# Optimization experiments

Measured on AMD Instinct MI355X. Metric: run time of the kernel, lower is better.

Reference implementation:

```python
import jax, jax.numpy as jnp
import numpy as np

N, E, H, HEADS, NC, BLK = 100000, 1600000, 128, 4, 8192, 128

def _layernorm(x, g, b, eps=1e-5):
    m = jnp.mean(x, axis=-1, keepdims=True)
    v = jnp.var(x, axis=-1, keepdims=True)
    return (x - m) * jax.lax.rsqrt(v + eps) * g + b

def setup_inputs() -> dict:
    key = jax.random.key(0)
    ks = jax.random.split(key, 24)
    s = 0.05
    p = lambda k, shp: jax.random.normal(k, shp, jnp.float32) * s
    return {
        'x': jax.random.normal(ks[0], (N, H), jnp.float32),
        'ea': jax.random.normal(ks[1], (E, H), jnp.float32),
        # GINEConv edge linear (edge_dim -> hidden)
        'We': p(ks[2], (H, H)), 'be_': p(ks[3], (H,)),
        # GINEConv mlp: Linear(H,H) -> ReLU -> Linear(H,H)
        'W1': p(ks[4], (H, H)), 'b1': p(ks[5], (H,)),
        'W2': p(ks[6], (H, H)), 'b2': p(ks[7], (H,)),
        'ln1_g': jnp.ones((H,), jnp.float32), 'ln1_b': jnp.zeros((H,), jnp.float32),
        # MultiheadAttention packed qkv + out proj
        'in_w': p(ks[8], (3 * H, H)), 'in_b': p(ks[9], (3 * H,)),
        'out_w': p(ks[10], (H, H)), 'out_b': p(ks[11], (H,)),
        'ln2_g': jnp.ones((H,), jnp.float32), 'ln2_b': jnp.zeros((H,), jnp.float32),
        # FFN: Linear(H,2H) -> ReLU -> Linear(2H,H)
        'f1_w': p(ks[12], (2 * H, H)), 'f1_b': p(ks[13], (2 * H,)),
        'f2_w': p(ks[14], (H, 2 * H)), 'f2_b': p(ks[15], (H,)),
        'ei': jax.random.randint(ks[16], (2, E), 0, N, jnp.int64),
        'chem_idx': jnp.arange(NC, dtype=jnp.int64),
        'B': BLK,
    }

def reference(x, ea, We, be_, W1, b1, W2, b2, ln1_g, ln1_b, in_w, in_b,
              out_w, out_b, ln2_g, ln2_b, f1_w, f1_b, f2_w, f2_b,
              ei, chem_idx, B):
    n = x.shape[0]
    # ---- GINEConv: out_i = mlp((1+eps)*x_i + sum_j relu(x_j + lin(e_ji))), eps=0 ----
    src, dst = ei[0], ei[1]
    msg = jax.nn.relu(x[src] + ea @ We.T + be_)          # [E, H]
    agg = jax.ops.segment_sum(msg, dst, num_segments=n)  # [N, H]
    h = agg + x
    h = jax.nn.relu(h @ W1.T + b1) @ W2.T + b2
    x = _layernorm(x + h, ln1_g, ln1_b)
    # ---- chunked self-attention over chem nodes (chunks of size B) ----
    xc = x[chem_idx].reshape(-1, B, x.shape[-1])         # [nc, B, H]
    nc, _, hid = xc.shape
    dh = hid // HEADS
    qkv = xc @ in_w.T + in_b                             # [nc, B, 3H]
    q, k, v = jnp.split(qkv, 3, axis=-1)
    sp = lambda t: t.reshape(nc, B, HEADS, dh)
    att = jax.nn.softmax(jnp.einsum('bqhd,bkhd->bhqk', sp(q), sp(k)) * (1.0 / np.sqrt(dh)).astype(np.float32), axis=-1)
    o = jnp.einsum('bhqk,bkhd->bqhd', att, sp(v)).reshape(nc, B, hid)
    xc = xc + (o @ out_w.T + out_b)                      # residual inside BlockMHA
    xc = xc.reshape(-1, hid)
    # ---- FFN on chem subset ----
    h2 = _layernorm(xc, ln2_g, ln2_b)
    xc = xc + (jax.nn.relu(h2 @ f1_w.T + f1_b) @ f2_w.T + f2_b)
    return x.at[chem_idx].set(xc)
```

## Files before the change

kernel.cpp:

```cpp
#include <hip/hip_runtime.h>
#include <hip/hip_bf16.h>
#include <math.h>

typedef __attribute__((ext_vector_type(8))) __bf16 bf16x8;
typedef __attribute__((ext_vector_type(4))) float f32x4;
typedef __attribute__((ext_vector_type(4))) unsigned short u16x4;

#define HD  128
#define LDP 136

__device__ __forceinline__ unsigned short f2bf(float f) {
  __bf16 h = (__bf16)f;
  union { __bf16 h; unsigned short u; } v; v.h = h; return v.u;
}
__device__ __forceinline__ float bf2f(unsigned short h) {
  union { unsigned u; float f; } v; v.u = ((unsigned)h) << 16; return v.f;
}

__device__ __forceinline__ int idx_at(const void* p, long long i, int is64) {
  if (is64) return (int)((const long long*)p)[i];
  return ((const int*)p)[i];
}

__device__ __forceinline__ void mfma_tile_128(const unsigned short* a_s,
                                              const unsigned short* w_s,
                                              int w, int l15, int lg,
                                              f32x4 acc[2][8]) {
#pragma unroll
  for (int kk = 0; kk < 4; ++kk) {
    bf16x8 a[2], b[8];
#pragma unroll
    for (int mt = 0; mt < 2; ++mt)
      a[mt] = *(const bf16x8*)&a_s[(w * 32 + mt * 16 + l15) * LDP + kk * 32 + lg * 8];
#pragma unroll
    for (int nt = 0; nt < 8; ++nt)
      b[nt] = *(const bf16x8*)&w_s[(nt * 16 + l15) * LDP + kk * 32 + lg * 8];
#pragma unroll
    for (int mt = 0; mt < 2; ++mt)
#pragma unroll
      for (int nt = 0; nt < 8; ++nt)
        acc[mt][nt] = __builtin_amdgcn_mfma_f32_16x16x32_bf16(a[mt], b[nt], acc[mt][nt], 0, 0, 0);
  }
}

__device__ __forceinline__ void mfma_tile_gb(const unsigned short* a_s,
                                             const unsigned short* Wb,
                                             int w, int l15, int lg,
                                             f32x4 acc[2][8]) {
#pragma unroll
  for (int kk = 0; kk < 4; ++kk) {
    bf16x8 a[2], b[8];
#pragma unroll
    for (int mt = 0; mt < 2; ++mt)
      a[mt] = *(const bf16x8*)&a_s[(w * 32 + mt * 16 + l15) * LDP + kk * 32 + lg * 8];
#pragma unroll
    for (int nt = 0; nt < 8; ++nt)
      b[nt] = *(const bf16x8*)&Wb[(nt * 16 + l15) * 128 + kk * 32 + lg * 8];
#pragma unroll
    for (int mt = 0; mt < 2; ++mt)
#pragma unroll
      for (int nt = 0; nt < 8; ++nt)
        acc[mt][nt] = __builtin_amdgcn_mfma_f32_16x16x32_bf16(a[mt], b[nt], acc[mt][nt], 0, 0, 0);
  }
}

__device__ __forceinline__ void stage_f32s(unsigned short* dst, const float* src,
                                           long long src_ld, int tid, int T) {
  for (int i = tid; i < 128 * 32; i += T) {
    int r = i >> 5, c = (i & 31) << 2;
    float4 f = *(const float4*)&src[(long long)r * src_ld + c];
    u16x4 h = { f2bf(f.x), f2bf(f.y), f2bf(f.z), f2bf(f.w) };
    *(u16x4*)&dst[r * LDP + c] = h;
  }
}

__global__ void detect_idx_kernel(const void* __restrict__ ei, int E, int N,
                                  int* __restrict__ flag) {
  if (threadIdx.x == 0 && blockIdx.x == 0) {
    const long long* p = (const long long*)ei;
    int is64 = 1;
    long long step = E / 64; if (step < 1) step = 1;
    for (int i = 0; i < 64; ++i) {
      long long v = p[i * step];
      if (v < 0 || v >= N) { is64 = 0; break; }
    }
    *flag = is64;
  }
}

__global__ __launch_bounds__(256) void conv_we_kernel(const float* __restrict__ We,
                                                      unsigned short* __restrict__ we_bf) {
  int i = blockIdx.x * 256 + threadIdx.x;
  if (i < 128 * 128) {
    int r = i >> 7, c = i & 127;
    we_bf[r * 136 + c] = f2bf(We[i]);
  }
}
__global__ __launch_bounds__(256) void conv_w_kernel(const float* __restrict__ W,
                                                     unsigned short* __restrict__ out,
                                                     int n) {
  int i = blockIdx.x * 256 + threadIdx.x;
  if (i < n) out[i] = f2bf(W[i]);
}
__global__ __launch_bounds__(256) void conv_x_kernel(const float* __restrict__ x,
                                                     unsigned short* __restrict__ xb,
                                                     long long n8) {
  long long i = blockIdx.x * 256LL + threadIdx.x;
  if (i < n8) {
    float4 f0 = *(const float4*)&x[i * 8];
    float4 f1 = *(const float4*)&x[i * 8 + 4];
    u16x4 h0 = { f2bf(f0.x), f2bf(f0.y), f2bf(f0.z), f2bf(f0.w) };
    u16x4 h1 = { f2bf(f1.x), f2bf(f1.y), f2bf(f1.z), f2bf(f1.w) };
    *(u16x4*)&xb[i * 8] = h0;
    *(u16x4*)&xb[i * 8 + 4] = h1;
  }
}

__global__ __launch_bounds__(256) void hist_kernel(const void* __restrict__ ei,
                                                   const int* __restrict__ flag,
                                                   int* __restrict__ deg, int E) {
  const int is64 = *flag;
  for (long long e = blockIdx.x * 256LL + threadIdx.x; e < E;
       e += (long long)gridDim.x * 256)
    atomicAdd(&deg[idx_at(ei, (long long)E + e, is64)], 1);
}

#define SCH 1024
__global__ __launch_bounds__(256) void scan_a(const int* __restrict__ deg,
                                              int* __restrict__ bsum, int N) {
  const int b = blockIdx.x, t = threadIdx.x;
  int p = 0;
#pragma unroll
  for (int k = 0; k < 4; ++k) {
    int idx = b * SCH + t * 4 + k;
    if (idx < N) p += deg[idx];
  }
  __shared__ int warr[4];
  for (int o = 32; o > 0; o >>= 1) p += __shfl_xor(p, o);
  if ((t & 63) == 0) warr[t >> 6] = p;
  __syncthreads();
  if (t == 0) bsum[b] = warr[0] + warr[1] + warr[2] + warr[3];
}
__global__ void scan_b(int* __restrict__ bsum, int* __restrict__ off, int NB, int N) {
  if (threadIdx.x == 0 && blockIdx.x == 0) {
    int run = 0;
    for (int b = 0; b < NB; ++b) { int t = bsum[b]; bsum[b] = run; run += t; }
    off[N] = run;
  }
}
__global__ __launch_bounds__(128) void scan_b2(int* __restrict__ bsum,
                                               int* __restrict__ off, int NB, int N) {
  __shared__ int arr[128];
  const int t = threadIdx.x;
  int v = (t < NB) ? bsum[t] : 0;
  arr[t] = v;
  __syncthreads();
  for (int s = 1; s < 128; s <<= 1) {
    int u = (t >= s) ? arr[t - s] : 0;
    __syncthreads();
    arr[t] += u;
    __syncthreads();
  }
  if (t < NB) bsum[t] = arr[t] - v;
  if (t == 0) off[N] = arr[127];
}
__global__ __launch_bounds__(256) void scan_c(const int* __restrict__ deg,
                                              const int* __restrict__ bsum,
                                              int* __restrict__ off,
                                              int* __restrict__ cursor, int N) {
  const int b = blockIdx.x, t = threadIdx.x;
  int d[4], s = 0;
#pragma unroll
  for (int k = 0; k < 4; ++k) {
    int idx = b * SCH + t * 4 + k;
    d[k] = (idx < N) ? deg[idx] : 0;
    s += d[k];
  }
  __shared__ int arr[256];
  arr[t] = s;
  __syncthreads();
  for (int stp = 1; stp < 256; stp <<= 1) {
    int v = (t >= stp) ? arr[t - stp] : 0;
    __syncthreads();
    arr[t] += v;
    __syncthreads();
  }
  int base = bsum[b] + arr[t] - s;
  int acc = 0;
#pragma unroll
  for (int k = 0; k < 4; ++k) {
    int idx = b * SCH + t * 4 + k;
    if (idx < N) { off[idx] = base + acc; cursor[idx] = base + acc; }
    acc += d[k];
  }
}

__global__ __launch_bounds__(256, 4) void edge_kernel9(
    const unsigned short* __restrict__ x_bf, const float* __restrict__ ea,
    const unsigned short* __restrict__ we_bf, const float* __restrict__ be,
    const void* __restrict__ ei, const int* __restrict__ flag,
    int* __restrict__ cursor, unsigned short* __restrict__ msg, int E) {
  __shared__ unsigned short we_s[128 * LDP];
  __shared__ int s_src[128];
  __shared__ int s_pos[128];
  const int tid = threadIdx.x;
  const long long e0 = (long long)blockIdx.x * 128;
  const int is64 = *flag;

  if (tid < 128) {
    long long e = e0 + tid;
    int s = 0, p = 0;
    if (e < E) {
      s = idx_at(ei, e, is64);
      int d = idx_at(ei, (long long)E + e, is64);
      p = atomicAdd(&cursor[d], 1);
    }
    s_src[tid] = s; s_pos[tid] = p;
  }

  const int lane = tid & 63, w = tid >> 6;
  const int l15 = lane & 15, lg = lane >> 4;

  float4 af[2][4][2];
#pragma unroll
  for (int mt = 0; mt < 2; ++mt) {
    long long row = e0 + w * 32 + mt * 16 + l15;
    const float* src = &ea[(row < E ? row : e0) * HD + lg * 8];
#pragma unroll
    for (int kk = 0; kk < 4; ++kk) {
      af[mt][kk][0] = *(const float4*)&src[kk * 32];
      af[mt][kk][1] = *(const float4*)&src[kk * 32 + 4];
    }
  }

  for (int i = tid; i < 2048; i += 256) {
    int r = i >> 4, c = (i & 15) << 3;
    *(float4*)&we_s[r * LDP + c] = *(const float4*)&we_bf[r * 136 + c];
  }

  bf16x8 a[2][4];
#pragma unroll
  for (int mt = 0; mt < 2; ++mt)
#pragma unroll
    for (int kk = 0; kk < 4; ++kk) {
      float4 f0 = af[mt][kk][0], f1 = af[mt][kk][1];
      bf16x8 t;
      t[0] = (__bf16)f0.x; t[1] = (__bf16)f0.y; t[2] = (__bf16)f0.z; t[3] = (__bf16)f0.w;
      t[4] = (__bf16)f1.x; t[5] = (__bf16)f1.y; t[6] = (__bf16)f1.z; t[7] = (__bf16)f1.w;
      a[mt][kk] = t;
    }
  __syncthreads();

  f32x4 acc[2][8];
#pragma unroll
  for (int mt = 0; mt < 2; ++mt)
#pragma unroll
    for (int nt = 0; nt < 8; ++nt) acc[mt][nt] = (f32x4){0.f, 0.f, 0.f, 0.f};

#pragma unroll
  for (int kk = 0; kk < 4; ++kk) {
    bf16x8 b[8];
#pragma unroll
    for (int nt = 0; nt < 8; ++nt)
      b[nt] = *(const bf16x8*)&we_s[(nt * 16 + l15) * LDP + kk * 32 + lg * 8];
#pragma unroll
    for (int mt = 0; mt < 2; ++mt)
#pragma unroll
      for (int nt = 0; nt < 8; ++nt)
        acc[mt][nt] = __builtin_amdgcn_mfma_f32_16x16x32_bf16(a[mt][kk], b[nt], acc[mt][nt], 0, 0, 0);
  }

  float bev[8];
#pragma unroll
  for (int nt = 0; nt < 8; ++nt) bev[nt] = be[nt * 16 + l15];
  __syncthreads();

#pragma unroll
  for (int mt = 0; mt < 2; ++mt)
#pragma unroll
    for (int r = 0; r < 4; ++r) {
      int m = w * 32 + mt * 16 + lg * 4 + r;
#pragma unroll
      for (int nt = 0; nt < 8; ++nt)
        we_s[m * LDP + nt * 16 + l15] = f2bf(acc[mt][nt][r] + bev[nt]);
    }
  __syncthreads();

  for (int i = tid; i < 128 * 16; i += 256) {
    int r = i >> 4, sg = i & 15;
    if (e0 + r >= E) continue;
    bf16x8 xv = *(const bf16x8*)&x_bf[(size_t)s_src[r] * HD + sg * 8];
    bf16x8 g = *(const bf16x8*)&we_s[r * LDP + sg * 8];
    u16x4 h0, h1;
#pragma unroll
    for (int k = 0; k < 4; ++k) {
      float v = (float)g[k] + (float)xv[k];
      h0[k] = f2bf(v > 0.f ? v : 0.f);
    }
#pragma unroll
    for (int k = 0; k < 4; ++k) {
      float v = (float)g[4 + k] + (float)xv[4 + k];
      h1[k] = f2bf(v > 0.f ? v : 0.f);
    }
    unsigned short* mp = &msg[(size_t)s_pos[r] * 128 + sg * 8];
    *(u16x4*)&mp[0] = h0;
    *(u16x4*)&mp[4] = h1;
  }
}

__global__ __launch_bounds__(256) void gather_kernel(
    const unsigned short* __restrict__ x_bf, const int* __restrict__ off,
    const unsigned short* __restrict__ msg, unsigned short* __restrict__ h_bf,
    int N) {
  const int tid = threadIdx.x;
  const int grp = tid >> 4, li = tid & 15;
  const long long row = (long long)blockIdx.x * 16 + grp;
  if (row >= N) return;
  const int co = li * 8;
  float a8[8];
  bf16x8 xv = *(const bf16x8*)&x_bf[row * HD + co];
#pragma unroll
  for (int k = 0; k < 8; ++k) a8[k] = (float)xv[k];
  const int j0 = off[row], j1 = off[row + 1];
  int j = j0;
  for (; j + 3 < j1; j += 4) {
    bf16x8 v0 = *(const bf16x8*)&msg[(size_t)j * 128 + co];
    bf16x8 v1 = *(const bf16x8*)&msg[(size_t)(j + 1) * 128 + co];
    bf16x8 v2 = *(const bf16x8*)&msg[(size_t)(j + 2) * 128 + co];
    bf16x8 v3 = *(const bf16x8*)&msg[(size_t)(j + 3) * 128 + co];
#pragma unroll
    for (int k = 0; k < 8; ++k)
      a8[k] += ((float)v0[k] + (float)v1[k]) + ((float)v2[k] + (float)v3[k]);
  }
  for (; j < j1; ++j) {
    bf16x8 v0 = *(const bf16x8*)&msg[(size_t)j * 128 + co];
#pragma unroll
    for (int k = 0; k < 8; ++k) a8[k] += (float)v0[k];
  }
  bf16x8 hv;
#pragma unroll
  for (int k = 0; k < 8; ++k) hv[k] = (__bf16)a8[k];
  *(bf16x8*)&h_bf[row * HD + co] = hv;
}

__global__ __launch_bounds__(256, 4) void mlp_kernel(
    const float* __restrict__ x, float* __restrict__ xo,
    const unsigned short* __restrict__ h_bf,
    const unsigned short* __restrict__ W1b, const float* __restrict__ b1,
    const unsigned short* __restrict__ W2b, const float* __restrict__ b2,
    const float* __restrict__ g1, const float* __restrict__ bt1, int N) {
  __shared__ unsigned short a_s[128 * LDP];
  const int tid = threadIdx.x;
  const long long r0 = (long long)blockIdx.x * 128;

  for (int i = tid; i < 2048; i += 256) {
    int r = i >> 4, c = (i & 15) << 3;
    long long gr = r0 + r;
    bf16x8 v;
    if (gr < N) v = *(const bf16x8*)&h_bf[gr * HD + c];
    else {
#pragma unroll
      for (int k = 0; k < 8; ++k) v[k] = (__bf16)0.f;
    }
    *(bf16x8*)&a_s[r * LDP + c] = v;
  }
  __syncthreads();

  const int lane = tid & 63, w = tid >> 6;
  const int l15 = lane & 15, lg = lane >> 4;
  f32x4 acc[2][8];
#pragma unroll
  for (int mt = 0; mt < 2; ++mt)
#pragma unroll
    for (int nt = 0; nt < 8; ++nt) acc[mt][nt] = (f32x4){0.f, 0.f, 0.f, 0.f};
  mfma_tile_gb(a_s, W1b, w, l15, lg, acc);
  __syncthreads();

#pragma unroll
  for (int mt = 0; mt < 2; ++mt)
#pragma unroll
    for (int r = 0; r < 4; ++r) {
      int m = w * 32 + mt * 16 + lg * 4 + r;
#pragma unroll
      for (int nt = 0; nt < 8; ++nt) {
        int n = nt * 16 + l15;
        float t = acc[mt][nt][r] + b1[n];
        a_s[m * LDP + n] = f2bf(t > 0.f ? t : 0.f);
      }
    }
  __syncthreads();

  f32x4 acc2[2][8];
#pragma unroll
  for (int mt = 0; mt < 2; ++mt)
#pragma unroll
    for (int nt = 0; nt < 8; ++nt) acc2[mt][nt] = (f32x4){0.f, 0.f, 0.f, 0.f};
  mfma_tile_gb(a_s, W2b, w, l15, lg, acc2);
  __syncthreads();

#pragma unroll
  for (int mt = 0; mt < 2; ++mt)
#pragma unroll
    for (int r = 0; r < 4; ++r) {
      int m = w * 32 + mt * 16 + lg * 4 + r;
      if (r0 + m < N) {
#pragma unroll
        for (int nt = 0; nt < 8; ++nt) {
          int n = nt * 16 + l15;
          a_s[m * LDP + n] = f2bf(x[(r0 + m) * HD + n] + acc2[mt][nt][r] + b2[n]);
        }
      }
    }
  __syncthreads();

  for (int row = w; row < 128; row += 4) {
    if (r0 + row >= N) continue;
    float v1 = bf2f(a_s[row * LDP + lane]), v2 = bf2f(a_s[row * LDP + 64 + lane]);
    float s = v1 + v2, sq = v1 * v1 + v2 * v2;
    for (int o = 32; o > 0; o >>= 1) { s += __shfl_xor(s, o); sq += __shfl_xor(sq, o); }
    float mean = s * (1.f / 128.f);
    float var = sq * (1.f / 128.f) - mean * mean;
    float rs = rsqrtf(var + 1e-5f);
    xo[(r0 + row) * HD + lane]      = (v1 - mean) * rs * g1[lane] + bt1[lane];
    xo[(r0 + row) * HD + 64 + lane] = (v2 - mean) * rs * g1[lane + 64] + bt1[lane + 64];
  }
}

__global__ __launch_bounds__(256) void edge_kernel(
    const float* __restrict__ x, const float* __restrict__ ea,
    const float* __restrict__ We, const float* __restrict__ be,
    const void* __restrict__ ei, const int* __restrict__ flag,
    float* __restrict__ agg, int E, int N) {
  __shared__ unsigned short ea_s[128 * LDP];
  __shared__ unsigned short we_s[128 * LDP];
  __shared__ int s_src[128];
  __shared__ int s_dst[128];
  const int tid = threadIdx.x;
  const long long e0 = (long long)blockIdx.x * 128;
  const int is64 = *flag;
  if (tid < 128) {
    long long e = e0 + tid;
    int s = 0, d = 0;
    if (e < E) { s = idx_at(ei, e, is64); d = idx_at(ei, (long long)E + e, is64); }
    s_src[tid] = s; s_dst[tid] = d;
  }
  for (int i = tid; i < 128 * 32; i += 256) {
    int r = i >> 5, c = (i & 31) << 2;
    float4 f = {0.f, 0.f, 0.f, 0.f};
    if (e0 + r < E) f = *(const float4*)&ea[(e0 + r) * HD + c];
    u16x4 h = { f2bf(f.x), f2bf(f.y), f2bf(f.z), f2bf(f.w) };
    *(u16x4*)&ea_s[r * LDP + c] = h;
    float4 g = *(const float4*)&We[r * HD + c];
    u16x4 hw = { f2bf(g.x), f2bf(g.y), f2bf(g.z), f2bf(g.w) };
    *(u16x4*)&we_s[r * LDP + c] = hw;
  }
  __syncthreads();
  const int lane = tid & 63, w = tid >> 6;
  const int l15 = lane & 15, lg = lane >> 4;
  f32x4 acc[2][8];
#pragma unroll
  for (int mt = 0; mt < 2; ++mt)
#pragma unroll
    for (int nt = 0; nt < 8; ++nt) acc[mt][nt] = (f32x4){0.f, 0.f, 0.f, 0.f};
  mfma_tile_128(ea_s, we_s, w, l15, lg, acc);
  float bev[8];
#pragma unroll
  for (int nt = 0; nt < 8; ++nt) bev[nt] = be[nt * 16 + l15];
#pragma unroll
  for (int mt = 0; mt < 2; ++mt) {
#pragma unroll
    for (int r = 0; r < 4; ++r) {
      int m = w * 32 + mt * 16 + lg * 4 + r;
      if (e0 + m >= E) continue;
      const float* xrow = x + (size_t)s_src[m] * HD;
      float* arow = agg + (size_t)s_dst[m] * HD;
#pragma unroll
      for (int nt = 0; nt < 8; ++nt) {
        int n = nt * 16 + l15;
        float val = acc[mt][nt][r] + bev[nt] + xrow[n];
        if (val > 0.f) unsafeAtomicAdd(&arow[n], val);
      }
    }
  }
}

__global__ __launch_bounds__(256) void node_kernel(
    const float* __restrict__ x, float* xo,
    const float* __restrict__ W1, const float* __restrict__ b1,
    const float* __restrict__ W2, const float* __restrict__ b2,
    const float* __restrict__ g1, const float* __restrict__ bt1, int N) {
  __shared__ char smem[2 * 128 * LDP * 2];
  unsigned short* a_s = (unsigned short*)smem;
  unsigned short* w_s = (unsigned short*)smem + 128 * LDP;
  float* y_s = (float*)smem;
  const int tid = threadIdx.x;
  const long long r0 = (long long)blockIdx.x * 128;
  for (int i = tid; i < 128 * 32; i += 256) {
    int r = i >> 5, c = (i & 31) << 2;
    float4 f = {0.f, 0.f, 0.f, 0.f};
    if (r0 + r < N) {
      float4 xa = *(const float4*)&x[(r0 + r) * HD + c];
      float4 ag = *(const float4*)&xo[(r0 + r) * HD + c];
      f.x = xa.x + ag.x; f.y = xa.y + ag.y; f.z = xa.z + ag.z; f.w = xa.w + ag.w;
    }
    u16x4 h = { f2bf(f.x), f2bf(f.y), f2bf(f.z), f2bf(f.w) };
    *(u16x4*)&a_s[r * LDP + c] = h;
    float4 g = *(const float4*)&W1[r * HD + c];
    u16x4 hw = { f2bf(g.x), f2bf(g.y), f2bf(g.z), f2bf(g.w) };
    *(u16x4*)&w_s[r * LDP + c] = hw;
  }
  __syncthreads();
  const int lane = tid & 63, w = tid >> 6;
  const int l15 = lane & 15, lg = lane >> 4;
  f32x4 acc[2][8];
#pragma unroll
  for (int mt = 0; mt < 2; ++mt)
#pragma unroll
    for (int nt = 0; nt < 8; ++nt) acc[mt][nt] = (f32x4){0.f, 0.f, 0.f, 0.f};
  mfma_tile_128(a_s, w_s, w, l15, lg, acc);
  __syncthreads();
#pragma unroll
  for (int mt = 0; mt < 2; ++mt)
#pragma unroll
    for (int r = 0; r < 4; ++r) {
      int m = w * 32 + mt * 16 + lg * 4 + r;
#pragma unroll
      for (int nt = 0; nt < 8; ++nt) {
        int n = nt * 16 + l15;
        float t = acc[mt][nt][r] + b1[n];
        a_s[m * LDP + n] = f2bf(t > 0.f ? t : 0.f);
      }
    }
  stage_f32s(w_s, W2, HD, tid, 256);
  __syncthreads();
  f32x4 acc2[2][8];
#pragma unroll
  for (int mt = 0; mt < 2; ++mt)
#pragma unroll
    for (int nt = 0; nt < 8; ++nt) acc2[mt][nt] = (f32x4){0.f, 0.f, 0.f, 0.f};
  mfma_tile_128(a_s, w_s, w, l15, lg, acc2);
  __syncthreads();
#pragma unroll
  for (int mt = 0; mt < 2; ++mt)
#pragma unroll
    for (int r = 0; r < 4; ++r) {
      int m = w * 32 + mt * 16 + lg * 4 + r;
      if (r0 + m < N) {
#pragma unroll
        for (int nt = 0; nt < 8; ++nt) {
          int n = nt * 16 + l15;
          y_s[m * 132 + n] = x[(r0 + m) * HD + n] + acc2[mt][nt][r] + b2[n];
        }
      }
    }
  __syncthreads();
  for (int row = w; row < 128; row += 4) {
    if (r0 + row >= N) continue;
    float v1 = y_s[row * 132 + lane], v2 = y_s[row * 132 + 64 + lane];
    float s = v1 + v2, sq = v1 * v1 + v2 * v2;
    for (int o = 32; o > 0; o >>= 1) { s += __shfl_xor(s, o); sq += __shfl_xor(sq, o); }
    float mean = s * (1.f / 128.f);
    float var = sq * (1.f / 128.f) - mean * mean;
    float rs = rsqrtf(var + 1e-5f);
    xo[(r0 + row) * HD + lane]      = (v1 - mean) * rs * g1[lane] + bt1[lane];
    xo[(r0 + row) * HD + 64 + lane] = (v2 - mean) * rs * g1[lane + 64] + bt1[lane + 64];
  }
}

__global__ __launch_bounds__(256) void qkv_kernel(
    const float* __restrict__ xo, const float* __restrict__ in_w,
    const float* __restrict__ in_b, const void* __restrict__ chem,
    const int* __restrict__ flag, float* __restrict__ qkv) {
  __shared__ unsigned short a_s[128 * LDP];
  __shared__ unsigned short w_s[128 * LDP];
  __shared__ int s_row[128];
  const int tid = threadIdx.x;
  const int chunk = blockIdx.x, sec = blockIdx.y;
  const int is64 = *flag;
  if (tid < 128) s_row[tid] = idx_at(chem, (long long)chunk * 128 + tid, is64);
  __syncthreads();
  for (int i = tid; i < 128 * 32; i += 256) {
    int r = i >> 5, c = (i & 31) << 2;
    float4 f = *(const float4*)&xo[(size_t)s_row[r] * HD + c];
    u16x4 h = { f2bf(f.x), f2bf(f.y), f2bf(f.z), f2bf(f.w) };
    *(u16x4*)&a_s[r * LDP + c] = h;
    float4 g = *(const float4*)&in_w[(size_t)(sec * 128 + r) * HD + c];
    u16x4 hw = { f2bf(g.x), f2bf(g.y), f2bf(g.z), f2bf(g.w) };
    *(u16x4*)&w_s[r * LDP + c] = hw;
  }
  __syncthreads();
  const int lane = tid & 63, w = tid >> 6;
  const int l15 = lane & 15, lg = lane >> 4;
  f32x4 acc[2][8];
#pragma unroll
  for (int mt = 0; mt < 2; ++mt)
#pragma unroll
    for (int nt = 0; nt < 8; ++nt) acc[mt][nt] = (f32x4){0.f, 0.f, 0.f, 0.f};
  mfma_tile_128(a_s, w_s, w, l15, lg, acc);
#pragma unroll
  for (int mt = 0; mt < 2; ++mt)
#pragma unroll
    for (int r = 0; r < 4; ++r) {
      int m = w * 32 + mt * 16 + lg * 4 + r;
#pragma unroll
      for (int nt = 0; nt < 8; ++nt) {
        int n = nt * 16 + l15;
        qkv[(size_t)(chunk * 128 + m) * 384 + sec * 128 + n] = acc[mt][nt][r] + in_b[sec * 128 + n];
      }
    }
}

__global__ __launch_bounds__(128) void attn_kernel(const float* __restrict__ qkv,
                                                   float* __restrict__ o) {
  __shared__ float k_s[128 * 32];
  __shared__ float v_s[128 * 32];
  const int tid = threadIdx.x;
  const int chunk = blockIdx.x, h = blockIdx.y;
  const float scale = 0.1767766952966369f;
  for (int i = tid; i < 128 * 32; i += 128) {
    int r = i >> 5, d = i & 31;
    k_s[i] = qkv[(size_t)(chunk * 128 + r) * 384 + 128 + h * 32 + d];
    v_s[i] = qkv[(size_t)(chunk * 128 + r) * 384 + 256 + h * 32 + d];
  }
  float qr[32];
  const int m = tid;
#pragma unroll
  for (int d = 0; d < 32; ++d)
    qr[d] = qkv[(size_t)(chunk * 128 + m) * 384 + h * 32 + d] * scale;
  __syncthreads();
  float mx = -1e30f, sm = 0.f;
  for (int j = 0; j < 128; ++j) {
    float s = 0.f;
#pragma unroll
    for (int d = 0; d < 32; ++d) s += qr[d] * k_s[j * 32 + d];
    if (s > mx) { sm = sm * __expf(mx - s); mx = s; }
    sm += __expf(s - mx);
  }
  const float inv = 1.f / sm;
  float ov[32];
#pragma unroll
  for (int d = 0; d < 32; ++d) ov[d] = 0.f;
  for (int j = 0; j < 128; ++j) {
    float s = 0.f;
#pragma unroll
    for (int d = 0; d < 32; ++d) s += qr[d] * k_s[j * 32 + d];
    float p = __expf(s - mx) * inv;
#pragma unroll
    for (int d = 0; d < 32; ++d) ov[d] += p * v_s[j * 32 + d];
  }
#pragma unroll
  for (int d = 0; d < 32; ++d)
    o[(size_t)(chunk * 128 + m) * HD + h * 32 + d] = ov[d];
}

__global__ __launch_bounds__(256) void oproj_kernel(
    const float* __restrict__ xo, const float* __restrict__ o,
    const float* __restrict__ Wo, const float* __restrict__ bo,
    const float* __restrict__ g2, const float* __restrict__ bt2,
    const void* __restrict__ chem, const int* __restrict__ flag,
    float* __restrict__ xc2, unsigned short* __restrict__ h2b) {
  __shared__ char smem[2 * 128 * LDP * 2];
  unsigned short* a_s = (unsigned short*)smem;
  unsigned short* w_s = (unsigned short*)smem + 128 * LDP;
  float* y_s = (float*)smem;
  __shared__ int s_row[128];
  const int tid = threadIdx.x;
  const int chunk = blockIdx.x;
  const int is64 = *flag;
  if (tid < 128) s_row[tid] = idx_at(chem, (long long)chunk * 128 + tid, is64);
  stage_f32s(a_s, o + (size_t)chunk * 128 * HD, HD, tid, 256);
  stage_f32s(w_s, Wo, HD, tid, 256);
  __syncthreads();
  const int lane = tid & 63, w = tid >> 6;
  const int l15 = lane & 15, lg = lane >> 4;
  f32x4 acc[2][8];
#pragma unroll
  for (int mt = 0; mt < 2; ++mt)
#pragma unroll
    for (int nt = 0; nt < 8; ++nt) acc[mt][nt] = (f32x4){0.f, 0.f, 0.f, 0.f};
  mfma_tile_128(a_s, w_s, w, l15, lg, acc);
  __syncthreads();
#pragma unroll
  for (int mt = 0; mt < 2; ++mt)
#pragma unroll
    for (int r = 0; r < 4; ++r) {
      int m = w * 32 + mt * 16 + lg * 4 + r;
#pragma unroll
      for (int nt = 0; nt < 8; ++nt) {
        int n = nt * 16 + l15;
        y_s[m * 132 + n] = xo[(size_t)s_row[m] * HD + n] + acc[mt][nt][r] + bo[n];
      }
    }
  __syncthreads();
  for (int row = w; row < 128; row += 4) {
    float v1 = y_s[row * 132 + lane], v2 = y_s[row * 132 + 64 + lane];
    float s = v1 + v2, sq = v1 * v1 + v2 * v2;
    for (int o2 = 32; o2 > 0; o2 >>= 1) { s += __shfl_xor(s, o2); sq += __shfl_xor(sq, o2); }
    float mean = s * (1.f / 128.f);
    float var = sq * (1.f / 128.f) - mean * mean;
    float rs = rsqrtf(var + 1e-5f);
    size_t gi = (size_t)(chunk * 128 + row) * HD;
    xc2[gi + lane] = v1; xc2[gi + 64 + lane] = v2;
    h2b[gi + lane]      = f2bf((v1 - mean) * rs * g2[lane] + bt2[lane]);
    h2b[gi + 64 + lane] = f2bf((v2 - mean) * rs * g2[lane + 64] + bt2[lane + 64]);
  }
}

__global__ __launch_bounds__(256) void ffn1_kernel(
    const unsigned short* __restrict__ h2b, const float* __restrict__ f1w,
    const float* __restrict__ f1b, unsigned short* __restrict__ u) {
  __shared__ unsigned short a_s[128 * LDP];
  __shared__ unsigned short w_s[128 * LDP];
  const int tid = threadIdx.x;
  const int chunk = blockIdx.x, sec = blockIdx.y;
  for (int i = tid; i < 128 * 32; i += 256) {
    int r = i >> 5, c = (i & 31) << 2;
    *(u16x4*)&a_s[r * LDP + c] = *(const u16x4*)&h2b[(size_t)(chunk * 128 + r) * HD + c];
  }
  stage_f32s(w_s, f1w + (size_t)sec * 128 * HD, HD, tid, 256);
  __syncthreads();
  const int lane = tid & 63, w = tid >> 6;
  const int l15 = lane & 15, lg = lane >> 4;
  f32x4 acc[2][8];
#pragma unroll
  for (int mt = 0; mt < 2; ++mt)
#pragma unroll
    for (int nt = 0; nt < 8; ++nt) acc[mt][nt] = (f32x4){0.f, 0.f, 0.f, 0.f};
  mfma_tile_128(a_s, w_s, w, l15, lg, acc);
#pragma unroll
  for (int mt = 0; mt < 2; ++mt)
#pragma unroll
    for (int r = 0; r < 4; ++r) {
      int m = w * 32 + mt * 16 + lg * 4 + r;
#pragma unroll
      for (int nt = 0; nt < 8; ++nt) {
        int n = nt * 16 + l15;
        float t = acc[mt][nt][r] + f1b[sec * 128 + n];
        u[(size_t)(chunk * 128 + m) * 256 + sec * 128 + n] = f2bf(t > 0.f ? t : 0.f);
      }
    }
}

__global__ __launch_bounds__(256) void ffn2_kernel(
    const unsigned short* __restrict__ u, const float* __restrict__ f2w,
    const float* __restrict__ f2b, const float* __restrict__ xc2,
    const void* __restrict__ chem, const int* __restrict__ flag,
    float* __restrict__ out) {
  __shared__ unsigned short a_s[128 * LDP];
  __shared__ unsigned short w_s[128 * LDP];
  __shared__ int s_row[128];
  const int tid = threadIdx.x;
  const int chunk = blockIdx.x;
  const int is64 = *flag;
  if (tid < 128) s_row[tid] = idx_at(chem, (long long)chunk * 128 + tid, is64);
  const int lane = tid & 63, w = tid >> 6;
  const int l15 = lane & 15, lg = lane >> 4;
  f32x4 acc[2][8];
#pragma unroll
  for (int mt = 0; mt < 2; ++mt)
#pragma unroll
    for (int nt = 0; nt < 8; ++nt) acc[mt][nt] = (f32x4){0.f, 0.f, 0.f, 0.f};
  for (int half = 0; half < 2; ++half) {
    __syncthreads();
    for (int i = tid; i < 128 * 32; i += 256) {
      int r = i >> 5, c = (i & 31) << 2;
      *(u16x4*)&a_s[r * LDP + c] =
          *(const u16x4*)&u[(size_t)(chunk * 128 + r) * 256 + half * 128 + c];
      float4 g = *(const float4*)&f2w[(size_t)r * 256 + half * 128 + c];
      u16x4 hw = { f2bf(g.x), f2bf(g.y), f2bf(g.z), f2bf(g.w) };
      *(u16x4*)&w_s[r * LDP + c] = hw;
    }
    __syncthreads();
    mfma_tile_128(a_s, w_s, w, l15, lg, acc);
  }
#pragma unroll
  for (int mt = 0; mt < 2; ++mt)
#pragma unroll
    for (int r = 0; r < 4; ++r) {
      int m = w * 32 + mt * 16 + lg * 4 + r;
#pragma unroll
      for (int nt = 0; nt < 8; ++nt) {
        int n = nt * 16 + l15;
        float val = xc2[(size_t)(chunk * 128 + m) * HD + n] + acc[mt][nt][r] + f2b[n];
        out[(size_t)s_row[m] * HD + n] = val;
      }
    }
}

extern "C" void kernel_launch(void* const* d_in, const int* in_sizes, int n_in,
                              void* d_out, int out_size, void* d_ws, size_t ws_size,
                              hipStream_t stream) {
  const float* x    = (const float*)d_in[0];
  const float* ea   = (const float*)d_in[1];
  const float* We   = (const float*)d_in[2];
  const float* be   = (const float*)d_in[3];
  const float* W1   = (const float*)d_in[4];
  const float* b1   = (const float*)d_in[5];
  const float* W2   = (const float*)d_in[6];
  const float* b2   = (const float*)d_in[7];
  const float* g1   = (const float*)d_in[8];
  const float* bt1  = (const float*)d_in[9];
  const float* in_w = (const float*)d_in[10];
  const float* in_b = (const float*)d_in[11];
  const float* outw = (const float*)d_in[12];
  const float* outb = (const float*)d_in[13];
  const float* g2   = (const float*)d_in[14];
  const float* bt2  = (const float*)d_in[15];
  const float* f1w  = (const float*)d_in[16];
  const float* f1b  = (const float*)d_in[17];
  const float* f2w  = (const float*)d_in[18];
  const float* f2b  = (const float*)d_in[19];
  const void*  ei   = d_in[20];
  const void*  chem = d_in[21];
  const int N  = in_sizes[0] / HD;
  const int E  = in_sizes[1] / HD;
  const int NC = in_sizes[21];
  const int NB = (N + SCH - 1) / SCH;
  float* xo = (float*)d_out;

  char* ws = (char*)d_ws;
  size_t o = 0;
  auto alloc = [&](size_t bytes) { size_t p = o; o = (o + bytes + 255) & ~255ULL; return p; };
  size_t o_qkv  = alloc((size_t)NC * 384 * 4);
  size_t o_obuf = alloc((size_t)NC * 128 * 4);
  size_t o_xc2  = alloc((size_t)NC * 128 * 4);
  size_t o_h2b  = alloc((size_t)NC * 128 * 2);
  size_t o_ubuf = alloc((size_t)NC * 256 * 2);
  size_t o_flag = alloc(4);
  size_t o_webf = alloc(128 * 136 * 2);
  size_t o_w1b  = alloc(128 * 128 * 2);
  size_t o_w2b  = alloc(128 * 128 * 2);
  size_t o_xbf  = alloc((size_t)N * 128 * 2);
  size_t o_hbf  = alloc((size_t)N * 128 * 2);
  size_t o_deg  = alloc((size_t)N * 4);
  size_t o_off  = alloc((size_t)(N + 1) * 4);
  size_t o_cur  = alloc((size_t)N * 4);
  size_t o_bsum = alloc((size_t)NB * 4);
  size_t o_msg  = alloc((size_t)E * 128 * 2);
  size_t need = o;

  float*          qkv  = (float*)(ws + o_qkv);
  float*          obuf = (float*)(ws + o_obuf);
  float*          xc2  = (float*)(ws + o_xc2);
  unsigned short* h2b  = (unsigned short*)(ws + o_h2b);
  unsigned short* ubuf = (unsigned short*)(ws + o_ubuf);
  int*            flag = (int*)(ws + o_flag);
  unsigned short* webf = (unsigned short*)(ws + o_webf);
  unsigned short* w1b  = (unsigned short*)(ws + o_w1b);
  unsigned short* w2b  = (unsigned short*)(ws + o_w2b);
  unsigned short* xbf  = (unsigned short*)(ws + o_xbf);
  unsigned short* hbf  = (unsigned short*)(ws + o_hbf);
  int*            deg  = (int*)(ws + o_deg);
  int*            off  = (int*)(ws + o_off);
  int*            cur  = (int*)(ws + o_cur);
  int*            bsum = (int*)(ws + o_bsum);
  unsigned short* msg  = (unsigned short*)(ws + o_msg);

  detect_idx_kernel<<<1, 64, 0, stream>>>(ei, E, N, flag);

  if (ws_size >= need) {
    hipMemsetAsync(deg, 0, (size_t)N * 4, stream);
    conv_x_kernel<<<dim3((N * 16 + 255) / 256), 256, 0, stream>>>(x, xbf, (long long)N * 16);
    hist_kernel<<<dim3(1024), 256, 0, stream>>>(ei, flag, deg, E);
    scan_a<<<dim3(NB), 256, 0, stream>>>(deg, bsum, N);
    if (NB <= 128) scan_b2<<<1, 128, 0, stream>>>(bsum, off, NB, N);
    else           scan_b<<<1, 64, 0, stream>>>(bsum, off, NB, N);
    scan_c<<<dim3(NB), 256, 0, stream>>>(deg, bsum, off, cur, N);
    conv_we_kernel<<<dim3(64), 256, 0, stream>>>(We, webf);
    conv_w_kernel<<<dim3(64), 256, 0, stream>>>(W1, w1b, 128 * 128);
    conv_w_kernel<<<dim3(64), 256, 0, stream>>>(W2, w2b, 128 * 128);
    edge_kernel9<<<dim3((E + 127) / 128), 256, 0, stream>>>(xbf, ea, webf, be, ei,
                                                            flag, cur, msg, E);
    gather_kernel<<<dim3((N + 15) / 16), 256, 0, stream>>>(xbf, off, msg, hbf, N);
    mlp_kernel<<<dim3((N + 127) / 128), 256, 0, stream>>>(x, xo, hbf, w1b, b1, w2b,
                                                          b2, g1, bt1, N);
  } else {
    hipMemsetAsync(xo, 0, (size_t)N * HD * sizeof(float), stream);
    edge_kernel<<<dim3((E + 127) / 128), 256, 0, stream>>>(x, ea, We, be, ei, flag, xo, E, N);
    node_kernel<<<dim3((N + 127) / 128), 256, 0, stream>>>(x, xo, W1, b1, W2, b2, g1, bt1, N);
  }

  const int ncs = NC / 128;
  qkv_kernel<<<dim3(ncs, 3), 256, 0, stream>>>(xo, in_w, in_b, chem, flag, qkv);
  attn_kernel<<<dim3(ncs, 4), 128, 0, stream>>>(qkv, obuf);
  oproj_kernel<<<dim3(ncs), 256, 0, stream>>>(xo, obuf, outw, outb, g2, bt2, chem, flag, xc2, h2b);
  ffn1_kernel<<<dim3(ncs, 2), 256, 0, stream>>>(h2b, f1w, f1b, ubuf);
  ffn2_kernel<<<dim3(ncs), 256, 0, stream>>>(ubuf, f2w, f2b, xc2, chem, flag, xo);
}
```

Before: 732.7 us.

## Write edge messages contiguously and gather through a sorted edge-id permutation

Moves the atomic slot assignment out of the edge kernel into a separate scatter kernel that records edge ids in CSR order. The edge kernel now writes messages contiguously in original edge order instead of scattering each row to its CSR slot. The gather kernel reads messages indirectly through the edge-id array. Writes become coalesced but gather reads become random, and the change adds an extra kernel plus a 4-byte-per-edge index array.

Result: slower. 803.2 us (+9.6%).

```diff
diff --git a/kernel.cpp b/kernel.cpp
--- a/kernel.cpp
+++ b/kernel.cpp
@@ -195,27 +195,32 @@
   }
 }
 
-__global__ __launch_bounds__(256, 4) void edge_kernel9(
+__global__ __launch_bounds__(256) void scatter_eid_kernel(
+    const void* __restrict__ ei, const int* __restrict__ flag,
+    int* __restrict__ cursor, int* __restrict__ eid, int E) {
+  const int is64 = *flag;
+  for (long long e = blockIdx.x * 256LL + threadIdx.x; e < E;
+       e += (long long)gridDim.x * 256) {
+    int d = idx_at(ei, (long long)E + e, is64);
+    int pos = atomicAdd(&cursor[d], 1);
+    eid[pos] = (int)e;
+  }
+}
+
+__global__ __launch_bounds__(256, 4) void edge_kernel10(
     const unsigned short* __restrict__ x_bf, const float* __restrict__ ea,
     const unsigned short* __restrict__ we_bf, const float* __restrict__ be,
     const void* __restrict__ ei, const int* __restrict__ flag,
-    int* __restrict__ cursor, unsigned short* __restrict__ msg, int E) {
+    unsigned short* __restrict__ msg, int E) {
   __shared__ unsigned short we_s[128 * LDP];
   __shared__ int s_src[128];
-  __shared__ int s_pos[128];
   const int tid = threadIdx.x;
   const long long e0 = (long long)blockIdx.x * 128;
   const int is64 = *flag;
 
   if (tid < 128) {
     long long e = e0 + tid;
-    int s = 0, p = 0;
-    if (e < E) {
-      s = idx_at(ei, e, is64);
-      int d = idx_at(ei, (long long)E + e, is64);
-      p = atomicAdd(&cursor[d], 1);
-    }
-    s_src[tid] = s; s_pos[tid] = p;
+    s_src[tid] = (e < E) ? idx_at(ei, e, is64) : 0;
   }
 
   const int lane = tid & 63, w = tid >> 6;
@@ -286,9 +291,10 @@
     }
   __syncthreads();
 
-  for (int i = tid; i < 128 * 16; i += 256) {
+  unsigned short* mbase = msg + (size_t)e0 * 128;
+  const int rows = (E - e0 < 128) ? (int)(E - e0) : 128;
+  for (int i = tid; i < rows * 16; i += 256) {
     int r = i >> 4, sg = i & 15;
-    if (e0 + r >= E) continue;
     bf16x8 xv = *(const bf16x8*)&x_bf[(size_t)s_src[r] * HD + sg * 8];
     bf16x8 g = *(const bf16x8*)&we_s[r * LDP + sg * 8];
     u16x4 h0, h1;
@@ -302,16 +308,16 @@
       float v = (float)g[4 + k] + (float)xv[4 + k];
       h1[k] = f2bf(v > 0.f ? v : 0.f);
     }
-    unsigned short* mp = &msg[(size_t)s_pos[r] * 128 + sg * 8];
+    unsigned short* mp = &mbase[(size_t)r * 128 + sg * 8];
     *(u16x4*)&mp[0] = h0;
     *(u16x4*)&mp[4] = h1;
   }
 }
 
-__global__ __launch_bounds__(256) void gather_kernel(
+__global__ __launch_bounds__(256) void gather_kernel10(
     const unsigned short* __restrict__ x_bf, const int* __restrict__ off,
-    const unsigned short* __restrict__ msg, unsigned short* __restrict__ h_bf,
-    int N) {
+    const int* __restrict__ eid, const unsigned short* __restrict__ msg,
+    unsigned short* __restrict__ h_bf, int N) {
   const int tid = threadIdx.x;
   const int grp = tid >> 4, li = tid & 15;
   const long long row = (long long)blockIdx.x * 16 + grp;
@@ -324,16 +330,17 @@
   const int j0 = off[row], j1 = off[row + 1];
   int j = j0;
   for (; j + 3 < j1; j += 4) {
-    bf16x8 v0 = *(const bf16x8*)&msg[(size_t)j * 128 + co];
-    bf16x8 v1 = *(const bf16x8*)&msg[(size_t)(j + 1) * 128 + co];
-    bf16x8 v2 = *(const bf16x8*)&msg[(size_t)(j + 2) * 128 + co];
-    bf16x8 v3 = *(const bf16x8*)&msg[(size_t)(j + 3) * 128 + co];
+    int e0 = eid[j], e1 = eid[j + 1], e2 = eid[j + 2], e3 = eid[j + 3];
+    bf16x8 v0 = *(const bf16x8*)&msg[(size_t)e0 * 128 + co];
+    bf16x8 v1 = *(const bf16x8*)&msg[(size_t)e1 * 128 + co];
+    bf16x8 v2 = *(const bf16x8*)&msg[(size_t)e2 * 128 + co];
+    bf16x8 v3 = *(const bf16x8*)&msg[(size_t)e3 * 128 + co];
 #pragma unroll
     for (int k = 0; k < 8; ++k)
       a8[k] += ((float)v0[k] + (float)v1[k]) + ((float)v2[k] + (float)v3[k]);
   }
   for (; j < j1; ++j) {
-    bf16x8 v0 = *(const bf16x8*)&msg[(size_t)j * 128 + co];
+    bf16x8 v0 = *(const bf16x8*)&msg[(size_t)eid[j] * 128 + co];
 #pragma unroll
     for (int k = 0; k < 8; ++k) a8[k] += (float)v0[k];
   }
@@ -836,6 +843,7 @@
   size_t o_off  = alloc((size_t)(N + 1) * 4);
   size_t o_cur  = alloc((size_t)N * 4);
   size_t o_bsum = alloc((size_t)NB * 4);
+  size_t o_eid  = alloc((size_t)E * 4);
   size_t o_msg  = alloc((size_t)E * 128 * 2);
   size_t need = o;
 
@@ -854,6 +862,7 @@
   int*            off  = (int*)(ws + o_off);
   int*            cur  = (int*)(ws + o_cur);
   int*            bsum = (int*)(ws + o_bsum);
+  int*            eid  = (int*)(ws + o_eid);
   unsigned short* msg  = (unsigned short*)(ws + o_msg);
 
   detect_idx_kernel<<<1, 64, 0, stream>>>(ei, E, N, flag);
@@ -866,12 +875,13 @@
     if (NB <= 128) scan_b2<<<1, 128, 0, stream>>>(bsum, off, NB, N);
     else           scan_b<<<1, 64, 0, stream>>>(bsum, off, NB, N);
     scan_c<<<dim3(NB), 256, 0, stream>>>(deg, bsum, off, cur, N);
+    scatter_eid_kernel<<<dim3(1024), 256, 0, stream>>>(ei, flag, cur, eid, E);
     conv_we_kernel<<<dim3(64), 256, 0, stream>>>(We, webf);
     conv_w_kernel<<<dim3(64), 256, 0, stream>>>(W1, w1b, 128 * 128);
     conv_w_kernel<<<dim3(64), 256, 0, stream>>>(W2, w2b, 128 * 128);
-    edge_kernel9<<<dim3((E + 127) / 128), 256, 0, stream>>>(xbf, ea, webf, be, ei,
-                                                            flag, cur, msg, E);
-    gather_kernel<<<dim3((N + 15) / 16), 256, 0, stream>>>(xbf, off, msg, hbf, N);
+    edge_kernel10<<<dim3((E + 127) / 128), 256, 0, stream>>>(xbf, ea, webf, be, ei,
+                                                             flag, msg, E);
+    gather_kernel10<<<dim3((N + 15) / 16), 256, 0, stream>>>(xbf, off, eid, msg, hbf, N);
     mlp_kernel<<<dim3((N + 127) / 128), 256, 0, stream>>>(x, xo, hbf, w1b, b1, w2b,
                                                           b2, g1, bt1, N);
   } else {
```
